# Kernel tuning notes

Measured on AMD Instinct MI355X. Metric: run time of the kernel, lower is better.

## Reference

```python
import jax, jax.numpy as jnp
import numpy as np

B, N = 512, 128          # molecules, max atoms
T = 10                   # NLSQ gradient-descent steps
STEP_EPS = 0.1
ALPHA, ALPHA_BASE = 5.0, 0.1
K_RANK, POWER_STEPS = 3, 10


def setup_inputs() -> dict:
    key = jax.random.key(0)
    k1, k2, k3, k4 = jax.random.split(key, 4)
    edge_pred = jax.random.normal(k1, (B, N, N, 2), dtype=jnp.float32)
    a = jax.random.randint(k2, (B, N, N), 0, 2)
    adj = ((a + a.transpose(0, 2, 1)) > 0).astype(jnp.int32)
    adj = adj * (1 - jnp.eye(N, dtype=jnp.int32))[None]  # symmetric, zero diagonal
    d_init = jnp.full((1,), 4.0, dtype=jnp.float32)      # learned scalar param
    u_init = jax.random.normal(k3, (B, N, 3), dtype=jnp.float32)   # power-iter inits (k=3 cols)
    x_noise = jax.random.normal(k4, (B, N, 3), dtype=jnp.float32)  # x_init additive noise
    return {"edge_pred": edge_pred, "adj": adj, "d_init": d_init,
            "u_init": u_init, "x_noise": x_noise}


def distances(X):
    # X: [B,N,3] -> [B,N,N]
    diff = X[:, None, :, :] - X[:, :, None, :]
    return jnp.sqrt(jnp.sum(diff * diff, axis=-1) + 0.01)


def distance_to_gram(D, mask):
    N_mol = jnp.sum(mask, axis=1)[:, 0].reshape(-1, 1, 1)
    D2 = D * D
    D_row = jnp.sum(D2, axis=1, keepdims=True) / N_mol
    D_col = jnp.sum(D2, axis=2, keepdims=True) / N_mol
    D_mean = jnp.sum(D2, axis=(1, 2), keepdims=True) / (N_mol * N_mol)
    return mask * (-0.5) * (D2 - D_row - D_col + D_mean)


def low_rank_approx_power(A, u_init):
    # A: [B,N,N]; u_init: [B,N,K_RANK] -> X: [B,N,K_RANK]
    A_lr = A
    cols = []
    for kx in range(K_RANK):
        u = u_init[..., kx:kx + 1]  # [B,N,1]
        for _ in range(POWER_STEPS):
            norm = jnp.sqrt(jnp.sum(u * u, axis=1, keepdims=True))
            u = u / jnp.maximum(norm, 1e-3)  # F.normalize(dim=1, eps=1e-3)
            u = jnp.matmul(A_lr, u)
        eig_sq = jnp.sum(u * u, axis=1, keepdims=True)
        u = u / jnp.power(eig_sq + 0.01, 0.25)
        cols.append(u)
        A_lr = A_lr - jnp.matmul(u, u.transpose(0, 2, 1))
    return jnp.concatenate(cols, axis=2)


def dist_nlsq(D, W, mask, u_init, x_noise):
    def objective(X):
        D_X = distances(X)
        U = jnp.sum(mask * W * jnp.square(D - D_X), axis=(1, 2)) / jnp.sum(mask, axis=(1, 2))
        return jnp.sum(U)

    gradfun = jax.grad(objective)
    Bg = distance_to_gram(D, mask)
    x0 = low_rank_approx_power(Bg, u_init) + x_noise

    def step(x, t):
        g = gradfun(x)
        dx = -STEP_EPS * g
        speed = jnp.sqrt(jnp.sum(dx * dx, axis=2, keepdims=True) + 0.001)
        alpha_t = ALPHA_BASE + (ALPHA - ALPHA_BASE) * ((T - t) / T)
        scale = alpha_t * jnp.tanh(speed / alpha_t) / speed
        return x + dx * scale, None

    x, _ = jax.lax.scan(step, x0, jnp.arange(T, dtype=jnp.float32))
    return x


def reference(edge_pred, adj, d_init, u_init, x_noise):
    diag_mask = adj.astype(jnp.float32)                      # [B,N,N], zero diagonal
    ep = edge_pred + edge_pred.transpose(0, 2, 1, 3)         # symmetrize
    preds = jax.nn.softplus(d_init + ep) * diag_mask[..., None]
    D, W = preds[..., 0], preds[..., 1]
    eye = jnp.eye(N, dtype=bool)[None]
    mask = jnp.where(eye, 1.0, diag_mask)                    # diagonal set to 1
    X = dist_nlsq(D, W, mask, u_init, x_noise)               # [B,N,3]
    return diag_mask * distances(X)
```

## Files before the change

### kernel.cpp

```cpp
#include <hip/hip_runtime.h>
#include <hip/hip_fp16.h>
#include <math.h>

#define NN   128
#define PSTR 132
#define NTH  512

__device__ __forceinline__ float sp_softplus(float x) {
    float p = __builtin_amdgcn_exp2f(fabsf(x) * -1.44269504f);
    float l = __builtin_amdgcn_logf(1.0f + p);
    return fmaxf(x, 0.0f) + 0.69314718f * l;
}
__device__ __forceinline__ float rdlane(float v, int l) {
    return __int_as_float(__builtin_amdgcn_readlane(__float_as_int(v), l));
}
__device__ __forceinline__ float rcpf(float x)  { return __builtin_amdgcn_rcpf(x); }
__device__ __forceinline__ float rsqf(float x)  { return __builtin_amdgcn_rsqf(x); }

__global__ void __launch_bounds__(NTH, 2)
ts_gcn_kernel(const float* __restrict__ edge_pred,
              const int*   __restrict__ adj,
              const float* __restrict__ d_init,
              const float* __restrict__ u_init,
              const float* __restrict__ x_noise,
              float* __restrict__ out)
{
    __shared__ __align__(16) float pool[NN * PSTR];
    __shared__ unsigned maskb[512];
    __shared__ int s_cntM, s_cntN0;

    float* scrA = pool;
    float* scrB = pool + 512;
    float* scrC = pool + 1024;
    float* Xx   = pool + 1536;
    float* Xy   = pool + 1664;
    float* Xz   = pool + 1792;
    float* r_s  = pool + 1920;

    const int b    = blockIdx.x;
    const int t    = threadIdx.x;
    const int lane = t & 63;
    const int i    = t & 127;
    const int q    = t >> 7;
    const int jb   = q * 32;
    const int lsel = jb & 63;
    const int hi6  = (t >> 6) & 1;

    const float dini = d_init[0];
    if (t == 0) { s_cntM = 0; s_cntN0 = 0; }

    const int4* adj4 = (const int4*)(adj + (size_t)b * 16384);
    #pragma unroll 4
    for (int k = 0; k < 8; ++k) {
        int e4 = t + k * 512;
        int4 v = adj4[e4];
        int ii = e4 >> 5, jj = (e4 & 31) * 4;
        float* p = &pool[ii * PSTR + jj];
        p[0] = __int_as_float(v.x); p[1] = __int_as_float(v.y);
        p[2] = __int_as_float(v.z); p[3] = __int_as_float(v.w);
    }
    __syncthreads();
    unsigned mword = 0;
    #pragma unroll
    for (int k = 0; k < 32; ++k) {
        int j = jb + k;
        int a = __float_as_int(pool[i * PSTR + j]) | __float_as_int(pool[j * PSTR + i]);
        if (a != 0 && i != j) mword |= (1u << k);
    }
    maskb[i * 4 + q] = mword;
    int cm = __popc(mword);
    #pragma unroll
    for (int off = 32; off; off >>= 1) cm += __shfl_xor(cm, off);
    if (lane == 0) atomicAdd(&s_cntM, cm);
    if (i == 0)    atomicAdd(&s_cntN0, __popc(mword));
    __syncthreads();

    const float4* ep4 = (const float4*)(edge_pred + (size_t)b * 32768);
    #pragma unroll 4
    for (int k = 0; k < 16; ++k) {
        int e2 = t + k * 512;
        float4 v = ep4[e2];
        int ii = e2 >> 6, jj = (e2 & 63) * 2;
        *(float2*)&pool[ii * PSTR + jj] = make_float2(v.x, v.z);
    }
    __syncthreads();
    float    Dfull[32];
    unsigned DWh[32];
    #pragma unroll
    for (int k = 0; k < 32; ++k) {
        int j = jb + k;
        float s = pool[i * PSTR + j] + pool[j * PSTR + i];
        float d = ((mword >> k) & 1) ? sp_softplus(dini + s) : 0.f;
        Dfull[k] = d;
        DWh[k] = (unsigned)__half_as_ushort(__float2half_rn(d));
    }
    __syncthreads();

    float rp = 0.f;
    #pragma unroll
    for (int k = 0; k < 32; ++k) rp = fmaf(Dfull[k], Dfull[k], rp);
    scrA[t] = rp;
    __syncthreads();
    if (t < NN)
        r_s[t] = (scrA[t] + scrA[t + 128]) + (scrA[t + 256] + scrA[t + 384]);
    __syncthreads();
    float mt = r_s[lane] + r_s[lane + 64];
    #pragma unroll
    for (int off = 32; off; off >>= 1) mt += __shfl_xor(mt, off);

    const float Nmol  = (float)(1 + s_cntN0);
    const float Minv  = 1.0f / (float)(128 + s_cntM);
    const float invN  = 1.0f / Nmol;
    const float cmean = mt * invN * invN;

    const float ri = r_s[i];
    float Bg[32];
    #pragma unroll
    for (int k = 0; k < 32; ++k) {
        int j = jb + k;
        float dv = Dfull[k];
        float v  = -0.5f * (dv * dv - ri * invN - r_s[j] * invN + cmean);
        bool msk = ((mword >> k) & 1) || (i == j);
        Bg[k] = msk ? v : 0.f;
    }
    __syncthreads();

    #pragma unroll 4
    for (int k = 0; k < 16; ++k) {
        int e2 = t + k * 512;
        float4 v = ep4[e2];
        int ii = e2 >> 6, jj = (e2 & 63) * 2;
        *(float2*)&pool[ii * PSTR + jj] = make_float2(v.y, v.w);
    }
    __syncthreads();
    #pragma unroll
    for (int k = 0; k < 32; ++k) {
        int j = jb + k;
        float s = pool[i * PSTR + j] + pool[j * PSTR + i];
        float w = ((mword >> k) & 1) ? sp_softplus(dini + s) : 0.f;
        DWh[k] |= ((unsigned)__half_as_ushort(__float2half_rn(w))) << 16;
    }
    __syncthreads();

    const float* ub = u_init  + (size_t)b * 384;
    const float* xb = x_noise + (size_t)b * 384;

    #pragma unroll 1
    for (int kx = 0; kx < 3; ++kx) {
        float ulo = ub[lane * 3 + kx];
        float uhi = ub[(lane + 64) * 3 + kx];
        float* rd = scrA; float* wr = scrB;
        #pragma unroll 1
        for (int s = 0; s < 10; ++s) {
            if (s) {
                ulo = (rd[lane]      + rd[lane + 128]) + (rd[lane + 256] + rd[lane + 384]);
                uhi = (rd[lane + 64] + rd[lane + 192]) + (rd[lane + 320] + rd[lane + 448]);
            }
            float n2 = fmaf(ulo, ulo, uhi * uhi);
            #pragma unroll
            for (int off = 32; off; off >>= 1) n2 += __shfl_xor(n2, off);
            float inv = rcpf(fmaxf(sqrtf(n2), 0.001f));
            float usel = (q < 2) ? ulo : uhi;
            float a0 = 0.f, a1 = 0.f;
            #pragma unroll
            for (int k = 0; k < 16; ++k) {
                a0 = fmaf(Bg[k],      rdlane(usel, lsel + k),      a0);
                a1 = fmaf(Bg[k + 16], rdlane(usel, lsel + k + 16), a1);
            }
            wr[t] = (a0 + a1) * inv;
            __syncthreads();
            float* tmp = rd; rd = wr; wr = tmp;
        }
        float ulo2 = (rd[lane]      + rd[lane + 128]) + (rd[lane + 256] + rd[lane + 384]);
        float uhi2 = (rd[lane + 64] + rd[lane + 192]) + (rd[lane + 320] + rd[lane + 448]);
        float e2 = fmaf(ulo2, ulo2, uhi2 * uhi2);
        #pragma unroll
        for (int off = 32; off; off >>= 1) e2 += __shfl_xor(e2, off);
        float esc  = rsqf(sqrtf(e2 + 0.01f));
        float ufi  = (hi6 ? uhi2 : ulo2) * esc;
        float uscl = ((q < 2) ? ulo2 : uhi2) * esc;
        #pragma unroll
        for (int k = 0; k < 32; ++k)
            Bg[k] = fmaf(-ufi, rdlane(uscl, lsel + k), Bg[k]);
        if (t < NN) {
            float* Xc = (kx == 0) ? Xx : (kx == 1) ? Xy : Xz;
            Xc[t] = ufi + xb[t * 3 + kx];
        }
        __syncthreads();
    }

    const float stepc = 0.4f * Minv;
    #pragma unroll 1
    for (int st = 0; st < 10; ++st) {
        float xix = Xx[i], xiy = Xy[i], xiz = Xz[i];
        float gx = 0.f, gy = 0.f, gz = 0.f;
        #pragma unroll
        for (int g = 0; g < 8; ++g) {
            float4 vx = *(const float4*)&Xx[jb + 4 * g];
            float4 vy = *(const float4*)&Xy[jb + 4 * g];
            float4 vz = *(const float4*)&Xz[jb + 4 * g];
            #pragma unroll
            for (int c = 0; c < 4; ++c) {
                int k = 4 * g + c;
                unsigned pw = DWh[k];
                float Dk = __half2float(__ushort_as_half((unsigned short)(pw & 0xffffu)));
                float Wk = __half2float(__ushort_as_half((unsigned short)(pw >> 16)));
                float jx = (c == 0) ? vx.x : (c == 1) ? vx.y : (c == 2) ? vx.z : vx.w;
                float jy = (c == 0) ? vy.x : (c == 1) ? vy.y : (c == 2) ? vy.z : vy.w;
                float jz = (c == 0) ? vz.x : (c == 1) ? vz.y : (c == 2) ? vz.z : vz.w;
                float dx = xix - jx, dy = xiy - jy, dz = xiz - jz;
                float d2 = fmaf(dx, dx, fmaf(dy, dy, fmaf(dz, dz, 0.01f)));
                float rv = rcpf(sqrtf(d2));
                float c2 = fmaf(Dk * rv, Wk, -Wk);
                gx = fmaf(c2, dx, gx);
                gy = fmaf(c2, dy, gy);
                gz = fmaf(c2, dz, gz);
            }
        }
        scrA[t] = gx; scrB[t] = gy; scrC[t] = gz;
        __syncthreads();
        if (t < NN) {
            float sx = (scrA[t] + scrA[t + 128]) + (scrA[t + 256] + scrA[t + 384]);
            float sy = (scrB[t] + scrB[t + 128]) + (scrB[t + 256] + scrB[t + 384]);
            float sz = (scrC[t] + scrC[t + 128]) + (scrC[t + 256] + scrC[t + 384]);
            float dxv = sx * stepc, dyv = sy * stepc, dzv = sz * stepc;
            float spd = sqrtf(fmaf(dxv, dxv, fmaf(dyv, dyv, fmaf(dzv, dzv, 0.001f))));
            float alpha = 0.1f + 4.9f * (float)(10 - st) * 0.1f;
            float z  = fminf(spd * rcpf(alpha), 20.0f);
            float e  = __builtin_amdgcn_exp2f(z * 2.88539008f);
            float th = (e - 1.0f) * rcpf(e + 1.0f);
            float scl = alpha * th * rcpf(spd);
            Xx[t] = fmaf(dxv, scl, Xx[t]);
            Xy[t] = fmaf(dyv, scl, Xy[t]);
            Xz[t] = fmaf(dzv, scl, Xz[t]);
        }
        __syncthreads();
    }

    float* ob = out + (size_t)b * 16384;
    #pragma unroll
    for (int k = 0; k < 8; ++k) {
        int e4 = t + k * 512;
        int ii = e4 >> 5, jjb = (e4 & 31) * 4;
        float xix = Xx[ii], xiy = Xy[ii], xiz = Xz[ii];
        float4 vx = *(const float4*)&Xx[jjb];
        float4 vy = *(const float4*)&Xy[jjb];
        float4 vz = *(const float4*)&Xz[jjb];
        unsigned mw = maskb[ii * 4 + (jjb >> 5)];
        float4 o;
        {
            float dx = xix - vx.x, dy = xiy - vy.x, dz = xiz - vz.x;
            float d2 = fmaf(dx, dx, fmaf(dy, dy, fmaf(dz, dz, 0.01f)));
            o.x = ((mw >> ((jjb + 0) & 31)) & 1) ? sqrtf(d2) : 0.f;
        }
        {
            float dx = xix - vx.y, dy = xiy - vy.y, dz = xiz - vz.y;
            float d2 = fmaf(dx, dx, fmaf(dy, dy, fmaf(dz, dz, 0.01f)));
            o.y = ((mw >> ((jjb + 1) & 31)) & 1) ? sqrtf(d2) : 0.f;
        }
        {
            float dx = xix - vx.z, dy = xiy - vy.z, dz = xiz - vz.z;
            float d2 = fmaf(dx, dx, fmaf(dy, dy, fmaf(dz, dz, 0.01f)));
            o.z = ((mw >> ((jjb + 2) & 31)) & 1) ? sqrtf(d2) : 0.f;
        }
        {
            float dx = xix - vx.w, dy = xiy - vy.w, dz = xiz - vz.w;
            float d2 = fmaf(dx, dx, fmaf(dy, dy, fmaf(dz, dz, 0.01f)));
            o.w = ((mw >> ((jjb + 3) & 31)) & 1) ? sqrtf(d2) : 0.f;
        }
        ((float4*)ob)[e4] = o;
    }
}

extern "C" void kernel_launch(void* const* d_in, const int* in_sizes, int n_in,
                              void* d_out, int out_size, void* d_ws, size_t ws_size,
                              hipStream_t stream) {
    const float* edge_pred = (const float*)d_in[0];
    const int*   adj       = (const int*)  d_in[1];
    const float* dinit     = (const float*)d_in[2];
    const float* u_init    = (const float*)d_in[3];
    const float* x_noise   = (const float*)d_in[4];
    float*       out       = (float*)d_out;

    ts_gcn_kernel<<<512, NTH, 0, stream>>>(edge_pred, adj, dinit, u_init, x_noise, out);
}
```

Measured before the change: 281.4 us.

## Keep D and W in fp32 registers and use LDS broadcast for power iteration

Stores D and W as separate fp32 register arrays instead of packed half pairs. The power-iteration matvec and deflation now read the vector from shared memory instead of using readlane broadcasts, which adds an extra barrier per step. The gradient loop uses rsq instead of rcp(sqrt), and the launch-bounds occupancy hint of 2 is dropped. This trades higher register pressure and possibly lower occupancy for less conversion work and scalar-lane traffic.

```diff
diff --git a/kernel.cpp b/kernel.cpp
--- a/kernel.cpp
+++ b/kernel.cpp
@@ -1,5 +1,4 @@
 #include <hip/hip_runtime.h>
-#include <hip/hip_fp16.h>
 #include <math.h>
 
 #define NN   128
@@ -11,13 +10,10 @@
     float l = __builtin_amdgcn_logf(1.0f + p);
     return fmaxf(x, 0.0f) + 0.69314718f * l;
 }
-__device__ __forceinline__ float rdlane(float v, int l) {
-    return __int_as_float(__builtin_amdgcn_readlane(__float_as_int(v), l));
-}
 __device__ __forceinline__ float rcpf(float x)  { return __builtin_amdgcn_rcpf(x); }
 __device__ __forceinline__ float rsqf(float x)  { return __builtin_amdgcn_rsqf(x); }
 
-__global__ void __launch_bounds__(NTH, 2)
+__global__ void __launch_bounds__(NTH)
 ts_gcn_kernel(const float* __restrict__ edge_pred,
               const int*   __restrict__ adj,
               const float* __restrict__ d_init,
@@ -27,6 +23,7 @@
 {
     __shared__ __align__(16) float pool[NN * PSTR];
     __shared__ unsigned maskb[512];
+    __shared__ float nrm2[2];
     __shared__ int s_cntM, s_cntN0;
 
     float* scrA = pool;
@@ -35,7 +32,8 @@
     float* Xx   = pool + 1536;
     float* Xy   = pool + 1664;
     float* Xz   = pool + 1792;
-    float* r_s  = pool + 1920;
+    float* u_s  = pool + 1920;
+    float* r_s  = pool + 2048;
 
     const int b    = blockIdx.x;
     const int t    = threadIdx.x;
@@ -43,8 +41,6 @@
     const int i    = t & 127;
     const int q    = t >> 7;
     const int jb   = q * 32;
-    const int lsel = jb & 63;
-    const int hi6  = (t >> 6) & 1;
 
     const float dini = d_init[0];
     if (t == 0) { s_cntM = 0; s_cntN0 = 0; }
@@ -84,21 +80,18 @@
         *(float2*)&pool[ii * PSTR + jj] = make_float2(v.x, v.z);
     }
     __syncthreads();
-    float    Dfull[32];
-    unsigned DWh[32];
+    float Dreg[32];
     #pragma unroll
     for (int k = 0; k < 32; ++k) {
         int j = jb + k;
         float s = pool[i * PSTR + j] + pool[j * PSTR + i];
-        float d = ((mword >> k) & 1) ? sp_softplus(dini + s) : 0.f;
-        Dfull[k] = d;
-        DWh[k] = (unsigned)__half_as_ushort(__float2half_rn(d));
+        Dreg[k] = ((mword >> k) & 1) ? sp_softplus(dini + s) : 0.f;
     }
     __syncthreads();
 
     float rp = 0.f;
     #pragma unroll
-    for (int k = 0; k < 32; ++k) rp = fmaf(Dfull[k], Dfull[k], rp);
+    for (int k = 0; k < 32; ++k) rp = fmaf(Dreg[k], Dreg[k], rp);
     scrA[t] = rp;
     __syncthreads();
     if (t < NN)
@@ -108,9 +101,8 @@
     #pragma unroll
     for (int off = 32; off; off >>= 1) mt += __shfl_xor(mt, off);
 
-    const float Nmol  = (float)(1 + s_cntN0);
     const float Minv  = 1.0f / (float)(128 + s_cntM);
-    const float invN  = 1.0f / Nmol;
+    const float invN  = 1.0f / (float)(1 + s_cntN0);
     const float cmean = mt * invN * invN;
 
     const float ri = r_s[i];
@@ -118,7 +110,7 @@
     #pragma unroll
     for (int k = 0; k < 32; ++k) {
         int j = jb + k;
-        float dv = Dfull[k];
+        float dv = Dreg[k];
         float v  = -0.5f * (dv * dv - ri * invN - r_s[j] * invN + cmean);
         bool msk = ((mword >> k) & 1) || (i == j);
         Bg[k] = msk ? v : 0.f;
@@ -133,12 +125,12 @@
         *(float2*)&pool[ii * PSTR + jj] = make_float2(v.y, v.w);
     }
     __syncthreads();
+    float Wreg[32];
     #pragma unroll
     for (int k = 0; k < 32; ++k) {
         int j = jb + k;
         float s = pool[i * PSTR + j] + pool[j * PSTR + i];
-        float w = ((mword >> k) & 1) ? sp_softplus(dini + s) : 0.f;
-        DWh[k] |= ((unsigned)__half_as_ushort(__float2half_rn(w))) << 16;
+        Wreg[k] = ((mword >> k) & 1) ? sp_softplus(dini + s) : 0.f;
     }
     __syncthreads();
 
@@ -147,44 +139,54 @@
 
     #pragma unroll 1
     for (int kx = 0; kx < 3; ++kx) {
-        float ulo = ub[lane * 3 + kx];
-        float uhi = ub[(lane + 64) * 3 + kx];
-        float* rd = scrA; float* wr = scrB;
         #pragma unroll 1
         for (int s = 0; s < 10; ++s) {
-            if (s) {
-                ulo = (rd[lane]      + rd[lane + 128]) + (rd[lane + 256] + rd[lane + 384]);
-                uhi = (rd[lane + 64] + rd[lane + 192]) + (rd[lane + 320] + rd[lane + 448]);
+            if (t < NN) {
+                float v = (s == 0) ? ub[t * 3 + kx]
+                        : (scrA[t] + scrA[t + 128]) + (scrA[t + 256] + scrA[t + 384]);
+                u_s[t] = v;
+                float p2 = v * v;
+                #pragma unroll
+                for (int off = 32; off; off >>= 1) p2 += __shfl_xor(p2, off);
+                if (lane == 0) nrm2[t >> 6] = p2;
             }
-            float n2 = fmaf(ulo, ulo, uhi * uhi);
+            __syncthreads();
+            float inv = rcpf(fmaxf(sqrtf(nrm2[0] + nrm2[1]), 0.001f));
+            float a = 0.f;
             #pragma unroll
-            for (int off = 32; off; off >>= 1) n2 += __shfl_xor(n2, off);
-            float inv = rcpf(fmaxf(sqrtf(n2), 0.001f));
-            float usel = (q < 2) ? ulo : uhi;
-            float a0 = 0.f, a1 = 0.f;
+            for (int g = 0; g < 8; ++g) {
+                float4 u4 = *(const float4*)&u_s[jb + 4 * g];
+                a = fmaf(Bg[4*g    ], u4.x, a);
+                a = fmaf(Bg[4*g + 1], u4.y, a);
+                a = fmaf(Bg[4*g + 2], u4.z, a);
+                a = fmaf(Bg[4*g + 3], u4.w, a);
+            }
+            scrA[t] = a * inv;
+            __syncthreads();
+        }
+        if (t < NN) {
+            float v = (scrA[t] + scrA[t + 128]) + (scrA[t + 256] + scrA[t + 384]);
+            u_s[t] = v;
+            float p2 = v * v;
             #pragma unroll
-            for (int k = 0; k < 16; ++k) {
-                a0 = fmaf(Bg[k],      rdlane(usel, lsel + k),      a0);
-                a1 = fmaf(Bg[k + 16], rdlane(usel, lsel + k + 16), a1);
-            }
-            wr[t] = (a0 + a1) * inv;
-            __syncthreads();
-            float* tmp = rd; rd = wr; wr = tmp;
-        }
-        float ulo2 = (rd[lane]      + rd[lane + 128]) + (rd[lane + 256] + rd[lane + 384]);
-        float uhi2 = (rd[lane + 64] + rd[lane + 192]) + (rd[lane + 320] + rd[lane + 448]);
-        float e2 = fmaf(ulo2, ulo2, uhi2 * uhi2);
+            for (int off = 32; off; off >>= 1) p2 += __shfl_xor(p2, off);
+            if (lane == 0) nrm2[t >> 6] = p2;
+        }
+        __syncthreads();
+        float e2  = nrm2[0] + nrm2[1];
+        float esc = rsqf(sqrtf(e2 + 0.01f));
+        float c   = u_s[i] * esc * esc;
         #pragma unroll
-        for (int off = 32; off; off >>= 1) e2 += __shfl_xor(e2, off);
-        float esc  = rsqf(sqrtf(e2 + 0.01f));
-        float ufi  = (hi6 ? uhi2 : ulo2) * esc;
-        float uscl = ((q < 2) ? ulo2 : uhi2) * esc;
-        #pragma unroll
-        for (int k = 0; k < 32; ++k)
-            Bg[k] = fmaf(-ufi, rdlane(uscl, lsel + k), Bg[k]);
+        for (int g = 0; g < 8; ++g) {
+            float4 u4 = *(const float4*)&u_s[jb + 4 * g];
+            Bg[4*g    ] = fmaf(-c, u4.x, Bg[4*g    ]);
+            Bg[4*g + 1] = fmaf(-c, u4.y, Bg[4*g + 1]);
+            Bg[4*g + 2] = fmaf(-c, u4.z, Bg[4*g + 2]);
+            Bg[4*g + 3] = fmaf(-c, u4.w, Bg[4*g + 3]);
+        }
         if (t < NN) {
             float* Xc = (kx == 0) ? Xx : (kx == 1) ? Xy : Xz;
-            Xc[t] = ufi + xb[t * 3 + kx];
+            Xc[t] = u_s[t] * esc + xb[t * 3 + kx];
         }
         __syncthreads();
     }
@@ -202,16 +204,13 @@
             #pragma unroll
             for (int c = 0; c < 4; ++c) {
                 int k = 4 * g + c;
-                unsigned pw = DWh[k];
-                float Dk = __half2float(__ushort_as_half((unsigned short)(pw & 0xffffu)));
-                float Wk = __half2float(__ushort_as_half((unsigned short)(pw >> 16)));
                 float jx = (c == 0) ? vx.x : (c == 1) ? vx.y : (c == 2) ? vx.z : vx.w;
                 float jy = (c == 0) ? vy.x : (c == 1) ? vy.y : (c == 2) ? vy.z : vy.w;
                 float jz = (c == 0) ? vz.x : (c == 1) ? vz.y : (c == 2) ? vz.z : vz.w;
                 float dx = xix - jx, dy = xiy - jy, dz = xiz - jz;
                 float d2 = fmaf(dx, dx, fmaf(dy, dy, fmaf(dz, dz, 0.01f)));
-                float rv = rcpf(sqrtf(d2));
-                float c2 = fmaf(Dk * rv, Wk, -Wk);
+                float rv = rsqf(d2);
+                float c2 = fmaf(Dreg[k] * rv, Wreg[k], -Wreg[k]);
                 gx = fmaf(c2, dx, gx);
                 gy = fmaf(c2, dy, gy);
                 gz = fmaf(c2, dz, gz);
@@ -248,26 +247,19 @@
         float4 vz = *(const float4*)&Xz[jjb];
         unsigned mw = maskb[ii * 4 + (jjb >> 5)];
         float4 o;
-        {
-            float dx = xix - vx.x, dy = xiy - vy.x, dz = xiz - vz.x;
-            float d2 = fmaf(dx, dx, fmaf(dy, dy, fmaf(dz, dz, 0.01f)));
-            o.x = ((mw >> ((jjb + 0) & 31)) & 1) ? sqrtf(d2) : 0.f;
-        }
-        {
-            float dx = xix - vx.y, dy = xiy - vy.y, dz = xiz - vz.y;
-            float d2 = fmaf(dx, dx, fmaf(dy, dy, fmaf(dz, dz, 0.01f)));
-            o.y = ((mw >> ((jjb + 1) & 31)) & 1) ? sqrtf(d2) : 0.f;
-        }
-        {
-            float dx = xix - vx.z, dy = xiy - vy.z, dz = xiz - vz.z;
-            float d2 = fmaf(dx, dx, fmaf(dy, dy, fmaf(dz, dz, 0.01f)));
-            o.z = ((mw >> ((jjb + 2) & 31)) & 1) ? sqrtf(d2) : 0.f;
-        }
-        {
-            float dx = xix - vx.w, dy = xiy - vy.w, dz = xiz - vz.w;
-            float d2 = fmaf(dx, dx, fmaf(dy, dy, fmaf(dz, dz, 0.01f)));
-            o.w = ((mw >> ((jjb + 3) & 31)) & 1) ? sqrtf(d2) : 0.f;
-        }
+        float dx, dy, dz, d2;
+        dx = xix - vx.x; dy = xiy - vy.x; dz = xiz - vz.x;
+        d2 = fmaf(dx, dx, fmaf(dy, dy, fmaf(dz, dz, 0.01f)));
+        o.x = ((mw >> ((jjb + 0) & 31)) & 1) ? sqrtf(d2) : 0.f;
+        dx = xix - vx.y; dy = xiy - vy.y; dz = xiz - vz.y;
+        d2 = fmaf(dx, dx, fmaf(dy, dy, fmaf(dz, dz, 0.01f)));
+        o.y = ((mw >> ((jjb + 1) & 31)) & 1) ? sqrtf(d2) : 0.f;
+        dx = xix - vx.z; dy = xiy - vy.z; dz = xiz - vz.z;
+        d2 = fmaf(dx, dx, fmaf(dy, dy, fmaf(dz, dz, 0.01f)));
+        o.z = ((mw >> ((jjb + 2) & 31)) & 1) ? sqrtf(d2) : 0.f;
+        dx = xix - vx.w; dy = xiy - vy.w; dz = xiz - vz.w;
+        d2 = fmaf(dx, dx, fmaf(dy, dy, fmaf(dz, dz, 0.01f)));
+        o.w = ((mw >> ((jjb + 3) & 31)) & 1) ? sqrtf(d2) : 0.f;
         ((float4*)ob)[e4] = o;
     }
 }
```

New measurement: 239.6 us. 14.9% less time.
